# Kernel tuning notes

Hardware: AMD Instinct MI355X
Metric: run time of the kernel (lower is better)

## Reference

```python
import jax, jax.numpy as jnp
import numpy as np

D_MODEL = 1024
N_HEADS = 16
D_K = D_MODEL // N_HEADS
D_FF = 4096
B, S = 2, 2048
LN_EPS = 1e-5
NEG_INF = -1e30  # finite stand-in for -inf; first (all-masked) row is overwritten by zeros anyway


def layer_norm(x, g, b):
    mu = jnp.mean(x, axis=-1, keepdims=True)
    var = jnp.mean(jnp.square(x - mu), axis=-1, keepdims=True)
    return (x - mu) * jax.lax.rsqrt(var + LN_EPS) * g + b


def setup_inputs() -> dict:
    key = jax.random.key(0)
    ks = jax.random.split(key, 16)
    sd = 0.02
    inp = {
        "query": jax.random.normal(ks[0], (B, S, D_MODEL), jnp.float32),
        "key": jax.random.normal(ks[1], (B, S, D_MODEL), jnp.float32),
        "values": jax.random.normal(ks[2], (B, S, D_MODEL), jnp.float32),
        "Wq": jax.random.normal(ks[3], (D_MODEL, D_MODEL), jnp.float32) * sd,
        "bq": jnp.zeros((D_MODEL,), jnp.float32),
        "Wk": jax.random.normal(ks[4], (D_MODEL, D_MODEL), jnp.float32) * sd,
        "bk": jnp.zeros((D_MODEL,), jnp.float32),
        "Wv": jax.random.normal(ks[5], (D_MODEL, D_MODEL), jnp.float32) * sd,
        "bv": jnp.zeros((D_MODEL,), jnp.float32),
        "Wo": jax.random.normal(ks[6], (D_MODEL, D_MODEL), jnp.float32) * sd,
        "bo": jnp.zeros((D_MODEL,), jnp.float32),
        "ln1_g": jnp.ones((D_MODEL,), jnp.float32),
        "ln1_b": jnp.zeros((D_MODEL,), jnp.float32),
        "W1": jax.random.normal(ks[7], (D_MODEL, D_FF), jnp.float32) * sd,
        "b1": jnp.zeros((D_FF,), jnp.float32),
        "W2": jax.random.normal(ks[8], (D_FF, D_MODEL), jnp.float32) * sd,
        "b2": jnp.zeros((D_MODEL,), jnp.float32),
        "ln2_g": jnp.ones((D_MODEL,), jnp.float32),
        "ln2_b": jnp.zeros((D_MODEL,), jnp.float32),
        "mask": 0,
    }
    return inp


def reference(query, key, values, Wq, bq, Wk, bk, Wv, bv, Wo, bo,
              ln1_g, ln1_b, W1, b1, W2, b2, ln2_g, ln2_b, mask):
    b, s, d = query.shape
    # projections -> [B, H, S, d_k]
    q = (query @ Wq + bq).reshape(b, s, N_HEADS, D_K).transpose(0, 2, 1, 3)
    k = (key @ Wk + bk).reshape(b, s, N_HEADS, D_K).transpose(0, 2, 1, 3)
    v = (values @ Wv + bv).reshape(b, s, N_HEADS, D_K).transpose(0, 2, 1, 3)
    # scores [B, H, S, S]
    scores = jnp.einsum("bhqd,bhkd->bhqk", q, k) / jnp.sqrt(jnp.float32(D_K))
    # torch: triu(ones, k=mask)==0 -> allowed iff j < i + mask
    i = jnp.arange(s)[:, None]
    j = jnp.arange(s)[None, :]
    allowed = j < (i + mask)
    scores = jnp.where(allowed, scores, NEG_INF)
    attn = jax.nn.softmax(scores, axis=-1)
    if mask == 0:
        # zero-pad trick: first query row (fully masked) is replaced by zeros
        attn = attn.at[:, :, 0, :].set(0.0)
    ctx = jnp.einsum("bhqk,bhkd->bhqd", attn, v)
    ctx = ctx.transpose(0, 2, 1, 3).reshape(b, s, d)
    attn_out = ctx @ Wo + bo
    x = layer_norm(query + attn_out, ln1_g, ln1_b)
    ffn = jax.nn.relu(x @ W1 + b1) @ W2 + b2
    out = layer_norm(x + ffn, ln2_g, ln2_b)
    return out
```

## Files before the change

kernel.cpp:

```cpp
#include <hip/hip_runtime.h>


typedef __attribute__((ext_vector_type(8))) __bf16 bf16x8;
typedef __attribute__((ext_vector_type(4))) float f32x4;

struct alignas(8)  S4 { short x, y, z, w; };
struct alignas(16) F4 { float x, y, z, w; };
struct alignas(16) I4 { int x, y, z, w; };

static __device__ __forceinline__ short f2bf(float f) {
  unsigned u = __float_as_uint(f);
  u += 0x7fff + ((u >> 16) & 1);
  return (short)(u >> 16);
}

static __device__ __forceinline__ void store_out(float* p, float v) { *p = v; }
static __device__ __forceinline__ void store_out(short* p, float v) { *p = f2bf(v); }

#define GLL16(g, l)                                                         \
  __builtin_amdgcn_global_load_lds(                                         \
      (__attribute__((address_space(1))) void*)(g),                         \
      (__attribute__((address_space(3))) void*)(l), 16, 0, 0)

__global__ __launch_bounds__(256) void cvt_bf16_kernel(
    const float* __restrict__ i0, const float* __restrict__ i1,
    const float* __restrict__ i2, short* __restrict__ o0,
    short* __restrict__ o1, short* __restrict__ o2) {
  int z = blockIdx.y;
  const float* in = z == 0 ? i0 : (z == 1 ? i1 : i2);
  short* out = z == 0 ? o0 : (z == 1 ? o1 : o2);
  int i = (blockIdx.x * 256 + threadIdx.x) * 4;
  F4 v = *(const F4*)(in + i);
  S4 o = { f2bf(v.x), f2bf(v.y), f2bf(v.z), f2bf(v.w) };
  *(S4*)(out + i) = o;
}

__global__ __launch_bounds__(256) void transpose_cvt_kernel(
    const float* __restrict__ Wq, const float* __restrict__ Wk,
    const float* __restrict__ Wv, const float* __restrict__ Wo,
    const float* __restrict__ W1, const float* __restrict__ W2,
    short* __restrict__ Wqt, short* __restrict__ Wkt,
    short* __restrict__ Wvt, short* __restrict__ Wot,
    short* __restrict__ W1t, short* __restrict__ W2t) {
  __shared__ float tile[64][65];
  int bid = blockIdx.x;
  const float* W; short* Wt; int K, N, kx, ny;
  if (bid < 1024) {
    int w = bid >> 8, t = bid & 255;
    W = w == 0 ? Wq : (w == 1 ? Wk : (w == 2 ? Wv : Wo));
    Wt = w == 0 ? Wqt : (w == 1 ? Wkt : (w == 2 ? Wvt : Wot));
    K = 1024; N = 1024; kx = t & 15; ny = t >> 4;
  } else if (bid < 2048) {
    int t = bid - 1024;
    W = W1; Wt = W1t; K = 1024; N = 4096; kx = t & 15; ny = t >> 4;
  } else {
    int t = bid - 2048;
    W = W2; Wt = W2t; K = 4096; N = 1024; kx = t & 63; ny = t >> 6;
  }
  int k0 = kx * 64, n0 = ny * 64;
  int tid = threadIdx.x;
  int rr = tid >> 4, cc = (tid & 15) * 4;
#pragma unroll
  for (int p = 0; p < 4; ++p) {
    int row = p * 16 + rr;
    F4 v = *(const F4*)&W[(long)(k0 + row) * N + n0 + cc];
    tile[row][cc] = v.x; tile[row][cc + 1] = v.y;
    tile[row][cc + 2] = v.z; tile[row][cc + 3] = v.w;
  }
  __syncthreads();
#pragma unroll
  for (int p = 0; p < 4; ++p) {
    int rn = p * 16 + rr;
    S4 o = { f2bf(tile[cc + 0][rn]), f2bf(tile[cc + 1][rn]),
             f2bf(tile[cc + 2][rn]), f2bf(tile[cc + 3][rn]) };
    *(S4*)&Wt[(long)(n0 + rn) * K + k0 + cc] = o;
  }
}

template <int OUT_MODE, bool RELU, bool RES, typename OT>
__device__ __forceinline__ void gemm_core(
    const short* __restrict__ A, const short* __restrict__ Bt,
    const float* __restrict__ bias, const float* __restrict__ res,
    OT* __restrict__ out, int M, int N, int K, int kBeg, int kEnd) {
  __shared__ __align__(16) short sA[128 * 64];
  __shared__ __align__(16) short sB[128 * 64];
  int tid = threadIdx.x;
  int lane = tid & 63, wave = tid >> 6;
  int col = lane & 15, quad = lane >> 4;
  int m0 = blockIdx.x * 128, n0 = blockIdx.y * 128;
  int wm = (wave & 1) * 64, wn = (wave >> 1) * 64;

  f32x4 acc[4][4] = {};

  for (int k0 = kBeg; k0 < kEnd; k0 += 64) {
    __syncthreads();
#pragma unroll
    for (int j = 0; j < 4; ++j) {
      int idx = j * 256 + tid;
      int row = idx >> 3, cp = idx & 7;
      int c = cp ^ (row & 7);
      const short* ga = A  + (long)(m0 + row) * K + k0 + c * 8;
      const short* gb = Bt + (long)(n0 + row) * K + k0 + c * 8;
      short* la = &sA[(j * 256 + (wave << 6)) * 8];
      short* lb = &sB[(j * 256 + (wave << 6)) * 8];
      GLL16(ga, la);
      GLL16(gb, lb);
    }
    __syncthreads();

#pragma unroll
    for (int kk = 0; kk < 2; ++kk) {
      bf16x8 a[4], b[4];
#pragma unroll
      for (int t = 0; t < 4; ++t) {
        int ra = wm + t * 16 + col;
        int ca = kk * 4 + quad;
        a[t] = *(const bf16x8*)&sA[ra * 64 + ((ca ^ (ra & 7)) << 3)];
        int rb = wn + t * 16 + col;
        b[t] = *(const bf16x8*)&sB[rb * 64 + ((ca ^ (rb & 7)) << 3)];
      }
#pragma unroll
      for (int t = 0; t < 4; ++t)
#pragma unroll
        for (int u = 0; u < 4; ++u)
          acc[t][u] = __builtin_amdgcn_mfma_f32_16x16x32_bf16(
              a[t], b[u], acc[t][u], 0, 0, 0);
    }
  }

#pragma unroll
  for (int t = 0; t < 4; ++t) {
#pragma unroll
    for (int u = 0; u < 4; ++u) {
      int Cc = n0 + wn + u * 16 + col;
      float bv = bias ? bias[Cc] : 0.f;
#pragma unroll
      for (int r = 0; r < 4; ++r) {
        int R = m0 + wm + t * 16 + quad * 4 + r;
        float v = acc[t][u][r] + bv;
        if (RES) v += res[(long)R * N + Cc];
        if (RELU) v = v > 0.f ? v : 0.f;
        if (OUT_MODE == 0) {
          store_out(&out[(long)R * N + Cc], v);
        } else {
          int bb = R >> 11, s = R & 2047, h = Cc >> 6, d = Cc & 63;
          store_out(&out[((long)((bb * 16 + h) * 2048 + s) << 6) + d], v);
        }
      }
    }
  }
}

template <int OUT_MODE, bool RELU, bool RES, typename OT>
__global__ __launch_bounds__(256) void gemm_bt(
    const short* __restrict__ A, const short* __restrict__ Bt,
    const float* __restrict__ bias, const float* __restrict__ res,
    OT* __restrict__ out, int M, int N, int K) {
  gemm_core<OUT_MODE, RELU, RES, OT>(A, Bt, bias, res, out, M, N, K, 0, K);
}

__global__ __launch_bounds__(256) void gemm_splitk(
    const short* __restrict__ A, const short* __restrict__ Bt,
    const float* __restrict__ bias, float* __restrict__ p0,
    float* __restrict__ p1, int M, int N, int K) {
  int z = blockIdx.z;
  float* out = z == 0 ? p0 : p1;
  const float* b = z == 0 ? bias : nullptr;
  int kc = K >> 1;
  gemm_core<0, false, false, float>(A, Bt, b, nullptr, out, M, N, K,
                                    z * kc, z * kc + kc);
}

__global__ __launch_bounds__(256) void gemm_qkv(
    const short* __restrict__ Aq, const short* __restrict__ Ak,
    const short* __restrict__ Av, const short* __restrict__ Btq,
    const short* __restrict__ Btk, const short* __restrict__ Btv,
    const float* __restrict__ bq, const float* __restrict__ bk,
    const float* __restrict__ bv, short* __restrict__ Qp,
    short* __restrict__ Kp, short* __restrict__ Vp) {
  int z = blockIdx.z;
  const short* A = z == 0 ? Aq : (z == 1 ? Ak : Av);
  const short* Bt = z == 0 ? Btq : (z == 1 ? Btk : Btv);
  const float* bias = z == 0 ? bq : (z == 1 ? bk : bv);
  short* out = z == 0 ? Qp : (z == 1 ? Kp : Vp);
  gemm_core<1, false, false, short>(A, Bt, bias, nullptr, out,
                                    4096, 1024, 1024, 0, 1024);
}

__global__ __launch_bounds__(256) void attn_kernel(
    const short* __restrict__ Q, const short* __restrict__ K,
    const short* __restrict__ V, const int* __restrict__ maskp,
    short* __restrict__ ctx) {
  __shared__ __align__(16) short sK[2][64 * 64];
  __shared__ __align__(16) int   sVt[2][64 * 32];
  __shared__ __align__(16) short sP[4 * 16 * 64];
  int tid = threadIdx.x, lane = tid & 63, wave = tid >> 6;
  int col = lane & 15, quad = lane >> 4;
  int pair = blockIdx.x, bh = blockIdx.y;
  int maskv = maskp[0];
  const long base = (long)bh * (2048 * 64);
  int b = bh >> 4, h = bh & 15;

  int kp = tid & 31, dg = tid >> 5, d0v = dg * 8;

  for (int pass = 0; pass < 2; ++pass) {
    int qt = pass ? (31 - pair) : pair;
    int i0 = qt * 64 + wave * 16;

    long jmax = (long)qt * 64 + 63 + maskv - 1;
    int tot = (jmax < 0) ? 0 : (int)(jmax >> 6) + 1;
    if (tot > 32) tot = 32;

    bf16x8 aQ[2];
#pragma unroll
    for (int kk = 0; kk < 2; ++kk)
      aQ[kk] = *(const bf16x8*)&Q[base + (long)(i0 + col) * 64 + kk * 32 + quad * 8];

    f32x4 o[4] = {};
    float lsum[4] = { 0.f, 0.f, 0.f, 0.f };

    if (tot > 0) {
#pragma unroll
      for (int j = 0; j < 2; ++j) {
        int idx = j * 256 + tid;
        int row = idx >> 3, cp = idx & 7;
        int c = cp ^ (row & 7);
        GLL16(K + base + (long)row * 64 + c * 8,
              &sK[0][(j * 256 + (wave << 6)) * 8]);
      }
      {
        union { I4 v; short s[8]; } u0, u1;
        u0.v = *(const I4*)&V[base + (long)(2 * kp) * 64 + d0v];
        u1.v = *(const I4*)&V[base + (long)(2 * kp + 1) * 64 + d0v];
#pragma unroll
        for (int j = 0; j < 8; ++j) {
          int d = d0v + j;
          int w = ((int)(unsigned short)u1.s[j] << 16) | (unsigned short)u0.s[j];
          sVt[0][d * 32 + ((((kp >> 2) ^ (d & 7)) << 2) | (kp & 3))] = w;
        }
      }
    }
    __syncthreads();

    for (int kt = 0; kt < tot; ++kt) {
      int cur = kt & 1, nxt = cur ^ 1;
      bool pf = (kt + 1 < tot);

      union { I4 v; short s[8]; } u0, u1;
      if (pf) {
#pragma unroll
        for (int j = 0; j < 2; ++j) {
          int idx = j * 256 + tid;
          int row = idx >> 3, cp = idx & 7;
          int c = cp ^ (row & 7);
          GLL16(K + base + (long)((kt + 1) * 64 + row) * 64 + c * 8,
                &sK[nxt][(j * 256 + (wave << 6)) * 8]);
        }
        u0.v = *(const I4*)&V[base + (long)((kt + 1) * 64 + 2 * kp) * 64 + d0v];
        u1.v = *(const I4*)&V[base + (long)((kt + 1) * 64 + 2 * kp + 1) * 64 + d0v];
      }

      f32x4 sc[4] = {};
#pragma unroll
      for (int kk = 0; kk < 2; ++kk) {
        int ca = kk * 4 + quad;
#pragma unroll
        for (int nt = 0; nt < 4; ++nt) {
          int rk = nt * 16 + col;
          bf16x8 bK = *(const bf16x8*)&sK[cur][rk * 64 + ((ca ^ (rk & 7)) << 3)];
          sc[nt] = __builtin_amdgcn_mfma_f32_16x16x32_bf16(aQ[kk], bK, sc[nt], 0, 0, 0);
        }
      }

      bool interior = (kt * 64 + 63) < (qt * 64 + maskv);
      if (interior) {
#pragma unroll
        for (int r = 0; r < 4; ++r) {
          int qr = quad * 4 + r;
#pragma unroll
          for (int nt = 0; nt < 4; ++nt) {
            float p = __expf(sc[nt][r] * 0.125f);
            lsum[r] += p;
            int k8 = nt * 2 + (col >> 3);
            sP[wave * 1024 + qr * 64 + (((k8 ^ (qr & 7)) << 3) | (col & 7))] =
                f2bf(p);
          }
        }
      } else {
#pragma unroll
        for (int r = 0; r < 4; ++r) {
          int i = i0 + quad * 4 + r;
          int qr = quad * 4 + r;
#pragma unroll
          for (int nt = 0; nt < 4; ++nt) {
            int j = kt * 64 + nt * 16 + col;
            float p = (j < i + maskv) ? __expf(sc[nt][r] * 0.125f) : 0.f;
            lsum[r] += p;
            int k8 = nt * 2 + (col >> 3);
            sP[wave * 1024 + qr * 64 + (((k8 ^ (qr & 7)) << 3) | (col & 7))] =
                f2bf(p);
          }
        }
      }

#pragma unroll
      for (int kk = 0; kk < 2; ++kk) {
        int ca = kk * 4 + quad;
        bf16x8 aP = *(const bf16x8*)&sP[wave * 1024 + col * 64 + ((ca ^ (col & 7)) << 3)];
#pragma unroll
        for (int dt = 0; dt < 4; ++dt) {
          int d = dt * 16 + col;
          bf16x8 bV = *(const bf16x8*)((const short*)sVt[cur] + d * 64 + ((ca ^ (d & 7)) << 3));
          o[dt] = __builtin_amdgcn_mfma_f32_16x16x32_bf16(aP, bV, o[dt], 0, 0, 0);
        }
      }

      if (pf) {
#pragma unroll
        for (int j = 0; j < 8; ++j) {
          int d = d0v + j;
          int w = ((int)(unsigned short)u1.s[j] << 16) | (unsigned short)u0.s[j];
          sVt[nxt][d * 32 + ((((kp >> 2) ^ (d & 7)) << 2) | (kp & 3))] = w;
        }
      }
      __syncthreads();
    }

#pragma unroll
    for (int r = 0; r < 4; ++r)
#pragma unroll
      for (int off = 1; off < 16; off <<= 1)
        lsum[r] += __shfl_xor(lsum[r], off);

#pragma unroll
    for (int r = 0; r < 4; ++r) {
      int i = i0 + quad * 4 + r;
      float inv = (lsum[r] > 0.f) ? 1.f / lsum[r] : 0.f;
      if (maskv == 0 && i == 0) inv = 0.f;
#pragma unroll
      for (int dt = 0; dt < 4; ++dt)
        ctx[(long)(b * 2048 + i) * 1024 + h * 64 + dt * 16 + col] =
            f2bf(o[dt][r] * inv);
    }
    __syncthreads();
  }
}

__global__ __launch_bounds__(256) void ln_comb_kernel(
    const float* __restrict__ p0, const float* __restrict__ p1,
    const float* __restrict__ res, const float* __restrict__ g,
    const float* __restrict__ b, float* __restrict__ outf,
    short* __restrict__ outb) {
  int r = blockIdx.x, tid = threadIdx.x;
  int lane = tid & 63, wave = tid >> 6;
  long off0 = (long)r * 1024;
  F4 a = ((const F4*)(p0 + off0))[tid];
  F4 c = ((const F4*)(p1 + off0))[tid];
  F4 d = ((const F4*)(res + off0))[tid];
  F4 v = { a.x + c.x + d.x, a.y + c.y + d.y, a.z + c.z + d.z, a.w + c.w + d.w };
  float s = v.x + v.y + v.z + v.w;
  float sq = v.x * v.x + v.y * v.y + v.z * v.z + v.w * v.w;
#pragma unroll
  for (int off = 1; off < 64; off <<= 1) {
    s += __shfl_xor(s, off);
    sq += __shfl_xor(sq, off);
  }
  __shared__ float rs[4], rq[4];
  if (lane == 0) { rs[wave] = s; rq[wave] = sq; }
  __syncthreads();
  s = rs[0] + rs[1] + rs[2] + rs[3];
  sq = rq[0] + rq[1] + rq[2] + rq[3];
  float mu = s * (1.0f / 1024.0f);
  float var = sq * (1.0f / 1024.0f) - mu * mu;
  float rstd = rsqrtf(var + 1e-5f);
  F4 gv = ((const F4*)g)[tid], bv = ((const F4*)b)[tid];
  F4 o;
  o.x = (v.x - mu) * rstd * gv.x + bv.x;
  o.y = (v.y - mu) * rstd * gv.y + bv.y;
  o.z = (v.z - mu) * rstd * gv.z + bv.z;
  o.w = (v.w - mu) * rstd * gv.w + bv.w;
  ((F4*)(outf + off0))[tid] = o;
  if (outb) {
    S4 ob = { f2bf(o.x), f2bf(o.y), f2bf(o.z), f2bf(o.w) };
    ((S4*)(outb + off0))[tid] = ob;
  }
}

extern "C" void kernel_launch(void* const* d_in, const int* in_sizes, int n_in,
                              void* d_out, int out_size, void* d_ws, size_t ws_size,
                              hipStream_t stream) {
  const float* query  = (const float*)d_in[0];
  const float* keyi   = (const float*)d_in[1];
  const float* values = (const float*)d_in[2];
  const float* Wq = (const float*)d_in[3];
  const float* bq = (const float*)d_in[4];
  const float* Wk = (const float*)d_in[5];
  const float* bk = (const float*)d_in[6];
  const float* Wv = (const float*)d_in[7];
  const float* bv = (const float*)d_in[8];
  const float* Wo = (const float*)d_in[9];
  const float* bo = (const float*)d_in[10];
  const float* ln1_g = (const float*)d_in[11];
  const float* ln1_b = (const float*)d_in[12];
  const float* W1 = (const float*)d_in[13];
  const float* b1 = (const float*)d_in[14];
  const float* W2 = (const float*)d_in[15];
  const float* b2 = (const float*)d_in[16];
  const float* ln2_g = (const float*)d_in[17];
  const float* ln2_b = (const float*)d_in[18];
  const int*   maskp = (const int*)d_in[19];
  float* out = (float*)d_out;

  char* ws = (char*)d_ws;
  const size_t MB = 1u << 20;
  short* q_bf = (short*)(ws + 0);
  short* k_bf = (short*)(ws + 8 * MB);
  short* v_bf = (short*)(ws + 16 * MB);
  short* ctx  = (short*)(ws + 24 * MB);
  short* Qp   = (short*)(ws + 32 * MB);
  short* Kp   = (short*)(ws + 40 * MB);
  short* Vp   = (short*)(ws + 48 * MB);
  short* Wqt  = (short*)(ws + 56 * MB);
  short* Wkt  = (short*)(ws + 58 * MB);
  short* Wvt  = (short*)(ws + 60 * MB);
  short* Wot  = (short*)(ws + 62 * MB);
  short* W1t  = (short*)(ws + 64 * MB);
  short* W2t  = (short*)(ws + 72 * MB);
  short* hbuf = (short*)(ws + 80 * MB);
  float* pWo0 = (float*)(ws + 0);
  float* pWo1 = (float*)(ws + 32 * MB);
  float* x_f32 = (float*)(ws + 16 * MB);
  short* x_bf  = (short*)(ws + 48 * MB);
  float* pF0 = (float*)(ws + 0);
  float* pF1 = (float*)(ws + 32 * MB);

  cvt_bf16_kernel<<<dim3(4096, 3), 256, 0, stream>>>(query, keyi, values,
                                                     q_bf, k_bf, v_bf);
  transpose_cvt_kernel<<<3072, 256, 0, stream>>>(Wq, Wk, Wv, Wo, W1, W2,
                                                 Wqt, Wkt, Wvt, Wot, W1t, W2t);
  gemm_qkv<<<dim3(32, 8, 3), 256, 0, stream>>>(q_bf, k_bf, v_bf,
                                               Wqt, Wkt, Wvt,
                                               bq, bk, bv, Qp, Kp, Vp);
  attn_kernel<<<dim3(16, 32), 256, 0, stream>>>(Qp, Kp, Vp, maskp, ctx);
  gemm_splitk<<<dim3(32, 8, 2), 256, 0, stream>>>(ctx, Wot, bo, pWo0, pWo1,
                                                  4096, 1024, 1024);
  ln_comb_kernel<<<4096, 256, 0, stream>>>(pWo0, pWo1, query, ln1_g, ln1_b,
                                           x_f32, x_bf);
  gemm_bt<0, true, false, short><<<dim3(32, 32), 256, 0, stream>>>(
      x_bf, W1t, b1, nullptr, hbuf, 4096, 4096, 1024);
  gemm_splitk<<<dim3(32, 8, 2), 256, 0, stream>>>(hbuf, W2t, b2, pF0, pF1,
                                                  4096, 1024, 4096);
  ln_comb_kernel<<<4096, 256, 0, stream>>>(pF0, pF1, x_f32, ln2_g, ln2_b,
                                           out, nullptr);

  (void)in_sizes; (void)n_in; (void)out_size; (void)ws_size;
}
```

Baseline: 412.2 us.

## Widen attention query tile to 128 rows with 8-wave blocks

The attention kernel now uses 512 threads (8 waves), each block covering a 128-row query tile, so every K/V tile staged in shared memory serves twice as many query rows. Each thread loads half as much K/V per tile, and the grid is reordered to (bh, pair) with 256 blocks instead of 512. The interior test is now per wave instead of per block, so waves that are fully past the causal edge skip masking. The cost is fewer blocks to fill the GPU, and waves covering the early rows of a tile sit idle through the extra key tiles that only the later rows need.

Result: no change. 407.3 us (-1.2%).

```diff
diff --git a/kernel.cpp b/kernel.cpp
--- a/kernel.cpp
+++ b/kernel.cpp
@@ -187,27 +187,28 @@
                                     4096, 1024, 1024, 0, 1024);
 }
 
-__global__ __launch_bounds__(256) void attn_kernel(
+__global__ __launch_bounds__(512) void attn_kernel(
     const short* __restrict__ Q, const short* __restrict__ K,
     const short* __restrict__ V, const int* __restrict__ maskp,
     short* __restrict__ ctx) {
   __shared__ __align__(16) short sK[2][64 * 64];
   __shared__ __align__(16) int   sVt[2][64 * 32];
-  __shared__ __align__(16) short sP[4 * 16 * 64];
-  int tid = threadIdx.x, lane = tid & 63, wave = tid >> 6;
+  __shared__ __align__(16) short sP[8 * 16 * 64];
+  int tid = threadIdx.x, wave = tid >> 6;
+  int lane = tid & 63;
   int col = lane & 15, quad = lane >> 4;
-  int pair = blockIdx.x, bh = blockIdx.y;
+  int bh = blockIdx.x, pair = blockIdx.y;
   int maskv = maskp[0];
   const long base = (long)bh * (2048 * 64);
   int b = bh >> 4, h = bh & 15;
 
-  int kp = tid & 31, dg = tid >> 5, d0v = dg * 8;
+  int kp = tid & 31, dg = tid >> 5, d0v = dg * 4;
 
   for (int pass = 0; pass < 2; ++pass) {
-    int qt = pass ? (31 - pair) : pair;
-    int i0 = qt * 64 + wave * 16;
-
-    long jmax = (long)qt * 64 + 63 + maskv - 1;
+    int qt = pass ? (15 - pair) : pair;
+    int i0 = qt * 128 + wave * 16;
+
+    long jmax = (long)qt * 128 + 127 + maskv - 1;
     int tot = (jmax < 0) ? 0 : (int)(jmax >> 6) + 1;
     if (tot > 32) tot = 32;
 
@@ -220,20 +221,18 @@
     float lsum[4] = { 0.f, 0.f, 0.f, 0.f };
 
     if (tot > 0) {
-#pragma unroll
-      for (int j = 0; j < 2; ++j) {
-        int idx = j * 256 + tid;
-        int row = idx >> 3, cp = idx & 7;
+      {
+        int row = tid >> 3, cp = tid & 7;
         int c = cp ^ (row & 7);
         GLL16(K + base + (long)row * 64 + c * 8,
-              &sK[0][(j * 256 + (wave << 6)) * 8]);
+              &sK[0][(wave << 6) * 8]);
       }
       {
-        union { I4 v; short s[8]; } u0, u1;
-        u0.v = *(const I4*)&V[base + (long)(2 * kp) * 64 + d0v];
-        u1.v = *(const I4*)&V[base + (long)(2 * kp + 1) * 64 + d0v];
-#pragma unroll
-        for (int j = 0; j < 8; ++j) {
+        union { S4 v; short s[4]; } u0, u1;
+        u0.v = *(const S4*)&V[base + (long)(2 * kp) * 64 + d0v];
+        u1.v = *(const S4*)&V[base + (long)(2 * kp + 1) * 64 + d0v];
+#pragma unroll
+        for (int j = 0; j < 4; ++j) {
           int d = d0v + j;
           int w = ((int)(unsigned short)u1.s[j] << 16) | (unsigned short)u0.s[j];
           sVt[0][d * 32 + ((((kp >> 2) ^ (d & 7)) << 2) | (kp & 3))] = w;
@@ -246,18 +245,14 @@
       int cur = kt & 1, nxt = cur ^ 1;
       bool pf = (kt + 1 < tot);
 
-      union { I4 v; short s[8]; } u0, u1;
+      union { S4 v; short s[4]; } u0, u1;
       if (pf) {
-#pragma unroll
-        for (int j = 0; j < 2; ++j) {
-          int idx = j * 256 + tid;
-          int row = idx >> 3, cp = idx & 7;
-          int c = cp ^ (row & 7);
-          GLL16(K + base + (long)((kt + 1) * 64 + row) * 64 + c * 8,
-                &sK[nxt][(j * 256 + (wave << 6)) * 8]);
-        }
-        u0.v = *(const I4*)&V[base + (long)((kt + 1) * 64 + 2 * kp) * 64 + d0v];
-        u1.v = *(const I4*)&V[base + (long)((kt + 1) * 64 + 2 * kp + 1) * 64 + d0v];
+        int row = tid >> 3, cp = tid & 7;
+        int c = cp ^ (row & 7);
+        GLL16(K + base + (long)((kt + 1) * 64 + row) * 64 + c * 8,
+              &sK[nxt][(wave << 6) * 8]);
+        u0.v = *(const S4*)&V[base + (long)((kt + 1) * 64 + 2 * kp) * 64 + d0v];
+        u1.v = *(const S4*)&V[base + (long)((kt + 1) * 64 + 2 * kp + 1) * 64 + d0v];
       }
 
       f32x4 sc[4] = {};
@@ -272,7 +267,7 @@
         }
       }
 
-      bool interior = (kt * 64 + 63) < (qt * 64 + maskv);
+      bool interior = (kt * 64 + 63) < (i0 + maskv);
       if (interior) {
 #pragma unroll
         for (int r = 0; r < 4; ++r) {
@@ -317,7 +312,7 @@
 
       if (pf) {
 #pragma unroll
-        for (int j = 0; j < 8; ++j) {
+        for (int j = 0; j < 4; ++j) {
           int d = d0v + j;
           int w = ((int)(unsigned short)u1.s[j] << 16) | (unsigned short)u0.s[j];
           sVt[nxt][d * 32 + ((((kp >> 2) ^ (d & 7)) << 2) | (kp & 3))] = w;
@@ -441,7 +436,7 @@
   gemm_qkv<<<dim3(32, 8, 3), 256, 0, stream>>>(q_bf, k_bf, v_bf,
                                                Wqt, Wkt, Wvt,
                                                bq, bk, bv, Qp, Kp, Vp);
-  attn_kernel<<<dim3(16, 32), 256, 0, stream>>>(Qp, Kp, Vp, maskp, ctx);
+  attn_kernel<<<dim3(32, 8), 512, 0, stream>>>(Qp, Kp, Vp, maskp, ctx);
   gemm_splitk<<<dim3(32, 8, 2), 256, 0, stream>>>(ctx, Wot, bo, pWo0, pWo1,
                                                   4096, 1024, 1024);
   ln_comb_kernel<<<4096, 256, 0, stream>>>(pWo0, pWo1, query, ln1_g, ln1_b,
```

## Enlarge attention query tile to 128 rows per block, dropping paired-pass scheme

Applied to the files above, without the earlier changes.

The attention kernel now processes a 128-row query tile per block (32 rows per wave, two 16-row groups) instead of two 64-row passes over paired tiles. Each K/V tile loaded into shared memory is reused by twice as many query rows, halving K/V global traffic and the V transpose work per query row. Heavy blocks are scheduled first via a reversed blockIdx.y, replacing the explicit pairing used for causal load balance. The cost is more registers for accumulators, double the sP shared memory, and only 512 blocks with uneven work per block.

New measurement: 415.5 us. About the same (+0.8%).

```diff
diff --git a/kernel.cpp b/kernel.cpp
--- a/kernel.cpp
+++ b/kernel.cpp
@@ -193,73 +193,76 @@
     short* __restrict__ ctx) {
   __shared__ __align__(16) short sK[2][64 * 64];
   __shared__ __align__(16) int   sVt[2][64 * 32];
-  __shared__ __align__(16) short sP[4 * 16 * 64];
+  __shared__ __align__(16) short sP[4 * 32 * 64];
   int tid = threadIdx.x, lane = tid & 63, wave = tid >> 6;
   int col = lane & 15, quad = lane >> 4;
-  int pair = blockIdx.x, bh = blockIdx.y;
+  int bh = blockIdx.x;
+  int qt = 15 - (int)blockIdx.y;
   int maskv = maskp[0];
   const long base = (long)bh * (2048 * 64);
   int b = bh >> 4, h = bh & 15;
+  int i0 = qt * 128 + wave * 32;
+
+  long jmax = (long)qt * 128 + 127 + maskv - 1;
+  int tot = (jmax < 0) ? 0 : (int)(jmax >> 6) + 1;
+  if (tot > 32) tot = 32;
+
+  bf16x8 aQ[2][2];
+#pragma unroll
+  for (int rg = 0; rg < 2; ++rg)
+#pragma unroll
+    for (int kk = 0; kk < 2; ++kk)
+      aQ[rg][kk] = *(const bf16x8*)&Q[base + (long)(i0 + rg * 16 + col) * 64 +
+                                      kk * 32 + quad * 8];
+
+  f32x4 o[2][4] = {};
+  float lsum[2][4] = {};
 
   int kp = tid & 31, dg = tid >> 5, d0v = dg * 8;
 
-  for (int pass = 0; pass < 2; ++pass) {
-    int qt = pass ? (31 - pair) : pair;
-    int i0 = qt * 64 + wave * 16;
-
-    long jmax = (long)qt * 64 + 63 + maskv - 1;
-    int tot = (jmax < 0) ? 0 : (int)(jmax >> 6) + 1;
-    if (tot > 32) tot = 32;
-
-    bf16x8 aQ[2];
-#pragma unroll
-    for (int kk = 0; kk < 2; ++kk)
-      aQ[kk] = *(const bf16x8*)&Q[base + (long)(i0 + col) * 64 + kk * 32 + quad * 8];
-
-    f32x4 o[4] = {};
-    float lsum[4] = { 0.f, 0.f, 0.f, 0.f };
-
-    if (tot > 0) {
+  if (tot > 0) {
+#pragma unroll
+    for (int j = 0; j < 2; ++j) {
+      int idx = j * 256 + tid;
+      int row = idx >> 3, cp = idx & 7;
+      int c = cp ^ (row & 7);
+      GLL16(K + base + (long)row * 64 + c * 8,
+            &sK[0][(j * 256 + (wave << 6)) * 8]);
+    }
+    {
+      union { I4 v; short s[8]; } u0, u1;
+      u0.v = *(const I4*)&V[base + (long)(2 * kp) * 64 + d0v];
+      u1.v = *(const I4*)&V[base + (long)(2 * kp + 1) * 64 + d0v];
+#pragma unroll
+      for (int j = 0; j < 8; ++j) {
+        int d = d0v + j;
+        int w = ((int)(unsigned short)u1.s[j] << 16) | (unsigned short)u0.s[j];
+        sVt[0][d * 32 + ((((kp >> 2) ^ (d & 7)) << 2) | (kp & 3))] = w;
+      }
+    }
+  }
+  __syncthreads();
+
+  for (int kt = 0; kt < tot; ++kt) {
+    int cur = kt & 1, nxt = cur ^ 1;
+    bool pf = (kt + 1 < tot);
+
+    union { I4 v; short s[8]; } u0, u1;
+    if (pf) {
 #pragma unroll
       for (int j = 0; j < 2; ++j) {
         int idx = j * 256 + tid;
         int row = idx >> 3, cp = idx & 7;
         int c = cp ^ (row & 7);
-        GLL16(K + base + (long)row * 64 + c * 8,
-              &sK[0][(j * 256 + (wave << 6)) * 8]);
-      }
-      {
-        union { I4 v; short s[8]; } u0, u1;
-        u0.v = *(const I4*)&V[base + (long)(2 * kp) * 64 + d0v];
-        u1.v = *(const I4*)&V[base + (long)(2 * kp + 1) * 64 + d0v];
-#pragma unroll
-        for (int j = 0; j < 8; ++j) {
-          int d = d0v + j;
-          int w = ((int)(unsigned short)u1.s[j] << 16) | (unsigned short)u0.s[j];
-          sVt[0][d * 32 + ((((kp >> 2) ^ (d & 7)) << 2) | (kp & 3))] = w;
-        }
-      }
-    }
-    __syncthreads();
-
-    for (int kt = 0; kt < tot; ++kt) {
-      int cur = kt & 1, nxt = cur ^ 1;
-      bool pf = (kt + 1 < tot);
-
-      union { I4 v; short s[8]; } u0, u1;
-      if (pf) {
-#pragma unroll
-        for (int j = 0; j < 2; ++j) {
-          int idx = j * 256 + tid;
-          int row = idx >> 3, cp = idx & 7;
-          int c = cp ^ (row & 7);
-          GLL16(K + base + (long)((kt + 1) * 64 + row) * 64 + c * 8,
-                &sK[nxt][(j * 256 + (wave << 6)) * 8]);
-        }
-        u0.v = *(const I4*)&V[base + (long)((kt + 1) * 64 + 2 * kp) * 64 + d0v];
-        u1.v = *(const I4*)&V[base + (long)((kt + 1) * 64 + 2 * kp + 1) * 64 + d0v];
-      }
-
+        GLL16(K + base + (long)((kt + 1) * 64 + row) * 64 + c * 8,
+              &sK[nxt][(j * 256 + (wave << 6)) * 8]);
+      }
+      u0.v = *(const I4*)&V[base + (long)((kt + 1) * 64 + 2 * kp) * 64 + d0v];
+      u1.v = *(const I4*)&V[base + (long)((kt + 1) * 64 + 2 * kp + 1) * 64 + d0v];
+    }
+
+#pragma unroll
+    for (int rg = 0; rg < 2; ++rg) {
       f32x4 sc[4] = {};
 #pragma unroll
       for (int kk = 0; kk < 2; ++kk) {
@@ -268,81 +271,88 @@
         for (int nt = 0; nt < 4; ++nt) {
           int rk = nt * 16 + col;
           bf16x8 bK = *(const bf16x8*)&sK[cur][rk * 64 + ((ca ^ (rk & 7)) << 3)];
-          sc[nt] = __builtin_amdgcn_mfma_f32_16x16x32_bf16(aQ[kk], bK, sc[nt], 0, 0, 0);
+          sc[nt] = __builtin_amdgcn_mfma_f32_16x16x32_bf16(aQ[rg][kk], bK,
+                                                           sc[nt], 0, 0, 0);
         }
       }
-
-      bool interior = (kt * 64 + 63) < (qt * 64 + maskv);
+      int irg = i0 + rg * 16;
+      bool interior = (kt * 64 + 63) < (irg + maskv);
       if (interior) {
 #pragma unroll
         for (int r = 0; r < 4; ++r) {
-          int qr = quad * 4 + r;
+          int qr = rg * 16 + quad * 4 + r;
 #pragma unroll
           for (int nt = 0; nt < 4; ++nt) {
             float p = __expf(sc[nt][r] * 0.125f);
-            lsum[r] += p;
+            lsum[rg][r] += p;
             int k8 = nt * 2 + (col >> 3);
-            sP[wave * 1024 + qr * 64 + (((k8 ^ (qr & 7)) << 3) | (col & 7))] =
+            sP[wave * 2048 + qr * 64 + (((k8 ^ (qr & 7)) << 3) | (col & 7))] =
                 f2bf(p);
           }
         }
       } else {
 #pragma unroll
         for (int r = 0; r < 4; ++r) {
-          int i = i0 + quad * 4 + r;
-          int qr = quad * 4 + r;
+          int i = irg + quad * 4 + r;
+          int qr = rg * 16 + quad * 4 + r;
 #pragma unroll
           for (int nt = 0; nt < 4; ++nt) {
             int j = kt * 64 + nt * 16 + col;
             float p = (j < i + maskv) ? __expf(sc[nt][r] * 0.125f) : 0.f;
-            lsum[r] += p;
+            lsum[rg][r] += p;
             int k8 = nt * 2 + (col >> 3);
-            sP[wave * 1024 + qr * 64 + (((k8 ^ (qr & 7)) << 3) | (col & 7))] =
+            sP[wave * 2048 + qr * 64 + (((k8 ^ (qr & 7)) << 3) | (col & 7))] =
                 f2bf(p);
           }
         }
       }
-
+    }
+
+#pragma unroll
+    for (int rg = 0; rg < 2; ++rg) {
 #pragma unroll
       for (int kk = 0; kk < 2; ++kk) {
         int ca = kk * 4 + quad;
-        bf16x8 aP = *(const bf16x8*)&sP[wave * 1024 + col * 64 + ((ca ^ (col & 7)) << 3)];
+        int pr = rg * 16 + col;
+        bf16x8 aP = *(const bf16x8*)&sP[wave * 2048 + pr * 64 +
+                                        ((ca ^ (pr & 7)) << 3)];
 #pragma unroll
         for (int dt = 0; dt < 4; ++dt) {
           int d = dt * 16 + col;
-          bf16x8 bV = *(const bf16x8*)((const short*)sVt[cur] + d * 64 + ((ca ^ (d & 7)) << 3));
-          o[dt] = __builtin_amdgcn_mfma_f32_16x16x32_bf16(aP, bV, o[dt], 0, 0, 0);
+          bf16x8 bV = *(const bf16x8*)((const short*)sVt[cur] + d * 64 +
+                                       ((ca ^ (d & 7)) << 3));
+          o[rg][dt] = __builtin_amdgcn_mfma_f32_16x16x32_bf16(aP, bV,
+                                                              o[rg][dt], 0, 0, 0);
         }
       }
-
-      if (pf) {
-#pragma unroll
-        for (int j = 0; j < 8; ++j) {
-          int d = d0v + j;
-          int w = ((int)(unsigned short)u1.s[j] << 16) | (unsigned short)u0.s[j];
-          sVt[nxt][d * 32 + ((((kp >> 2) ^ (d & 7)) << 2) | (kp & 3))] = w;
-        }
-      }
-      __syncthreads();
-    }
-
-#pragma unroll
-    for (int r = 0; r < 4; ++r)
+    }
+
+    if (pf) {
+#pragma unroll
+      for (int j = 0; j < 8; ++j) {
+        int d = d0v + j;
+        int w = ((int)(unsigned short)u1.s[j] << 16) | (unsigned short)u0.s[j];
+        sVt[nxt][d * 32 + ((((kp >> 2) ^ (d & 7)) << 2) | (kp & 3))] = w;
+      }
+    }
+    __syncthreads();
+  }
+
+#pragma unroll
+  for (int rg = 0; rg < 2; ++rg) {
+#pragma unroll
+    for (int r = 0; r < 4; ++r) {
 #pragma unroll
       for (int off = 1; off < 16; off <<= 1)
-        lsum[r] += __shfl_xor(lsum[r], off);
-
-#pragma unroll
-    for (int r = 0; r < 4; ++r) {
-      int i = i0 + quad * 4 + r;
-      float inv = (lsum[r] > 0.f) ? 1.f / lsum[r] : 0.f;
+        lsum[rg][r] += __shfl_xor(lsum[rg][r], off);
+      int i = i0 + rg * 16 + quad * 4 + r;
+      float inv = (lsum[rg][r] > 0.f) ? 1.f / lsum[rg][r] : 0.f;
       if (maskv == 0 && i == 0) inv = 0.f;
 #pragma unroll
       for (int dt = 0; dt < 4; ++dt)
         ctx[(long)(b * 2048 + i) * 1024 + h * 64 + dt * 16 + col] =
-            f2bf(o[dt][r] * inv);
-    }
-    __syncthreads();
+            f2bf(o[rg][dt][r] * inv);
+    }
   }
 }
 
@@ -441,7 +451,7 @@
   gemm_qkv<<<dim3(32, 8, 3), 256, 0, stream>>>(q_bf, k_bf, v_bf,
                                                Wqt, Wkt, Wvt,
                                                bq, bk, bv, Qp, Kp, Vp);
-  attn_kernel<<<dim3(16, 32), 256, 0, stream>>>(Qp, Kp, Vp, maskp, ctx);
+  attn_kernel<<<dim3(32, 16), 256, 0, stream>>>(Qp, Kp, Vp, maskp, ctx);
   gemm_splitk<<<dim3(32, 8, 2), 256, 0, stream>>>(ctx, Wot, bo, pWo0, pWo1,
                                                   4096, 1024, 1024);
   ln_comb_kernel<<<4096, 256, 0, stream>>>(pWo0, pWo1, query, ln1_g, ln1_b,
```
